# Kernel tuning notes

Measured on AMD Instinct MI355X. Metric: run time of the kernel, lower is better.

The kernel has to match this reference:

```python
import jax, jax.numpy as jnp
import numpy as np

COLLAPSE_FRAC = 4  # collapse F // 4 lowest-weight faces (target_size = 3/4 * F)


def setup_inputs() -> dict:
    key = jax.random.key(0)
    k1, k2, k3 = jax.random.split(key, 3)
    B, F, C, K = 8, 8192, 256, 4
    features = jax.random.normal(k1, (B, F, C), dtype=jnp.float32)
    adjacency = jax.random.randint(k2, (B, F, 3), 0, F).astype(jnp.int32)
    ring_k = jax.random.randint(k3, (B, F, K), 0, F).astype(jnp.int32)
    return {"features": features, "adjacency": adjacency, "ring_k": ring_k}


def _pool(features, adjacency, ring_k):
    # features:  [B, F, C] float   per-face features
    # adjacency: [B, F, 3] int     3 neighboring faces of each triangle
    # ring_k:    [B, F, K] int     k-ring neighborhood used for collapse weights
    B, F, C = features.shape
    K = ring_k.shape[-1]
    # ring-aggregated saliency weight per face (compute_weights analogue)
    rf = jnp.take_along_axis(
        features, ring_k.reshape(B, F * K)[:, :, None], axis=1
    ).reshape(B, F, K, C)                      # [B, F, K, C]
    w = jnp.linalg.norm(rf.mean(axis=2), axis=-1)  # [B, F]

    # select lowest-weight faces to collapse (idx/sorted analogue)
    P = F // COLLAPSE_FRAC
    _, collapse_idx = jax.lax.top_k(-w, P)      # [B, P]

    # gather the 3 region neighbors and the collapsed face features
    neighbors = jnp.take_along_axis(adjacency, collapse_idx[:, :, None], axis=1)  # [B, P, 3]
    cf = jnp.take_along_axis(features, collapse_idx[:, :, None], axis=1)          # [B, P, C]

    # scatter collapsed-face features into their 3 adjacent faces (update_features analogue)
    offs = (jnp.arange(B, dtype=jnp.int32) * F)[:, None, None]   # [B, 1, 1]
    seg = (neighbors + offs).reshape(-1)                          # [B*P*3]
    vals = jnp.broadcast_to(cf[:, :, None, :] / 3.0, (B, P, 3, C)).reshape(-1, C)
    scat = jax.ops.segment_sum(vals, seg, num_segments=B * F).reshape(B, F, C)
    cnt = jax.ops.segment_sum(
        jnp.ones(seg.shape, jnp.float32), seg, num_segments=B * F
    ).reshape(B, F, 1)
    merged = (features + scat) / (1.0 + cnt)

    # erase collapsed faces (erased / update_faces analogue; static shape, mask instead of compaction)
    erase_flat = (collapse_idx + offs[:, :, 0]).reshape(-1)
    keep = (
        jnp.ones((B * F,), jnp.float32).at[erase_flat].set(0.0).reshape(B, F, 1)
    )
    return merged * keep


def reference(features, adjacency, ring_k):
    return _pool(features, adjacency, ring_k)
```

## Files before the change

kernel.cpp:

```cpp
#include <hip/hip_runtime.h>
#include <stdint.h>

#define B 8
#define F 8192
#define C 256
#define K 4
#define P (F / 4)
#define CAP 16
#define NB 4096
#define BF (B * F)
#define CCAP 1024

typedef float f32x4 __attribute__((ext_vector_type(4)));

__device__ __forceinline__ int binOf(float v, float lo, float scale) {
    int bin = (int)((v - lo) * scale);
    return bin < 0 ? 0 : (bin > NB - 1 ? NB - 1 : bin);
}

__global__ __launch_bounds__(256) void kW(const float* __restrict__ feat,
                                          const int* __restrict__ ring,
                                          float* __restrict__ w,
                                          int* __restrict__ cnt,
                                          int* __restrict__ flag) {
    const int b     = blockIdx.x & 7;
    const int inner = blockIdx.x >> 3;
    const int wid   = b * F + inner * 4 + (threadIdx.x >> 6);
    const int lane  = threadIdx.x & 63;

    const int rbase = wid * K;
    const int r0 = ring[rbase + 0], r1 = ring[rbase + 1];
    const int r2 = ring[rbase + 2], r3 = ring[rbase + 3];
    const float4* f4 = (const float4*)feat;
    const size_t base = (size_t)b * F;
    const int    CW   = C / 4;
    const float4 v0 = f4[(base + r0) * CW + lane];
    const float4 v1 = f4[(base + r1) * CW + lane];
    const float4 v2 = f4[(base + r2) * CW + lane];
    const float4 v3 = f4[(base + r3) * CW + lane];

    float4 a;
    a.x = (v0.x + v1.x) + (v2.x + v3.x);
    a.y = (v0.y + v1.y) + (v2.y + v3.y);
    a.z = (v0.z + v1.z) + (v2.z + v3.z);
    a.w = (v0.w + v1.w) + (v2.w + v3.w);
    float s = (a.x * a.x + a.y * a.y + a.z * a.z + a.w * a.w) * 0.0625f;
#pragma unroll
    for (int off = 32; off > 0; off >>= 1) s += __shfl_down(s, off, 64);
    if (lane == 0) {
        w[wid]    = s;
        cnt[wid]  = 0;
        flag[wid] = 0;
    }
}

__global__ __launch_bounds__(256) void kFS(const float* __restrict__ w,
                                           const int* __restrict__ adj,
                                           int* __restrict__ flag,
                                           int* __restrict__ cnt,
                                           int* __restrict__ srcs) {
    __shared__ int h[NB];
    __shared__ unsigned long long carr[CCAP];
    __shared__ unsigned int redmn[4], redmx[4];
    __shared__ int wsum[4];
    __shared__ unsigned int slo, shi;
    __shared__ int sT, sR, scnt;
    const int g    = blockIdx.x;
    const int b    = g >> 5;
    const int gg   = g & 31;
    const int t    = threadIdx.x;
    const int lane = t & 63, wv = t >> 6;

    if (t == 0) scnt = 0;
    for (int i = t; i < NB; i += 256) h[i] = 0;

    float val[32];
    unsigned int mn = 0xFFFFFFFFu, mx = 0u;
#pragma unroll
    for (int k = 0; k < 32; ++k) {
        val[k] = w[b * F + k * 256 + t];
        const unsigned int u = __float_as_uint(val[k]);
        mn = mn < u ? mn : u;
        mx = mx > u ? mx : u;
    }
#pragma unroll
    for (int off = 32; off > 0; off >>= 1) {
        const unsigned int o1 = __shfl_xor(mn, off, 64); mn = mn < o1 ? mn : o1;
        const unsigned int o2 = __shfl_xor(mx, off, 64); mx = mx > o2 ? mx : o2;
    }
    if (lane == 0) { redmn[wv] = mn; redmx[wv] = mx; }
    __syncthreads();
    if (t == 0) {
        unsigned int a = redmn[0], c = redmx[0];
        for (int i = 1; i < 4; ++i) {
            a = a < redmn[i] ? a : redmn[i];
            c = c > redmx[i] ? c : redmx[i];
        }
        slo = a; shi = c;
    }
    __syncthreads();
    const float lo    = __uint_as_float(slo);
    const float hi    = __uint_as_float(shi);
    const float scale = (float)(NB - 2) / fmaxf(hi - lo, 1e-30f);

#pragma unroll
    for (int k = 0; k < 32; ++k) atomicAdd(&h[binOf(val[k], lo, scale)], 1);
    __syncthreads();

    int s = 0;
#pragma unroll
    for (int i = 0; i < 16; ++i) s += h[t * 16 + i];
    int incl = s;
#pragma unroll
    for (int off = 1; off < 64; off <<= 1) {
        const int u = __shfl_up(incl, off, 64);
        if (lane >= off) incl += u;
    }
    if (lane == 63) wsum[wv] = incl;
    __syncthreads();
    int add = 0;
    for (int i = 0; i < wv; ++i) add += wsum[i];
    const int inclT = incl + add;
    const int exclT = inclT - s;
    if (P - 1 >= exclT && P - 1 < inclT) {
        int c = exclT;
#pragma unroll
        for (int i = 0; i < 16; ++i) {
            const int bin = t * 16 + i;
            const int hv  = h[bin];
            if (P - 1 < c + hv) { sT = bin; sR = P - c; break; }
            c += hv;
        }
    }
    __syncthreads();
    const int T = sT, R = sR;

    const float myv = val[gg];
    const int face  = b * F + gg * 256 + t;
    if (binOf(myv, lo, scale) < T) {
        flag[face] = 1;
#pragma unroll
        for (int j = 0; j < 3; ++j) {
            const int n    = adj[(size_t)face * 3 + j];
            const int tgt  = b * F + n;
            const int slot = atomicAdd(&cnt[tgt], 1);
            if (slot < CAP) srcs[(size_t)tgt * CAP + slot] = face;
        }
    }

    if (gg == 0) {
#pragma unroll
        for (int k = 0; k < 32; ++k) {
            if (binOf(val[k], lo, scale) == T) {
                const int pos = atomicAdd(&scnt, 1);
                if (pos < CCAP)
                    carr[pos] = ((unsigned long long)__float_as_uint(val[k]) << 32) |
                                (uint32_t)(k * 256 + t);
            }
        }
        __syncthreads();
        const int n = scnt < CCAP ? scnt : CCAP;
        for (int i = t; i < n; i += 256) {
            const unsigned long long my = carr[i];
            int rank = 0;
            for (int j = 0; j < n; ++j) rank += (carr[j] < my) ? 1 : 0;
            if (rank < R) {
                const int tt = b * F + (int)(uint32_t)my;
                flag[tt] = 1;
#pragma unroll
                for (int j = 0; j < 3; ++j) {
                    const int nb   = adj[(size_t)tt * 3 + j];
                    const int tgt  = b * F + nb;
                    const int slot = atomicAdd(&cnt[tgt], 1);
                    if (slot < CAP) srcs[(size_t)tgt * CAP + slot] = tt;
                }
            }
        }
    }
}

__global__ __launch_bounds__(256) void kG(const float* __restrict__ feat,
                                          const int* __restrict__ cnt,
                                          const int* __restrict__ flag,
                                          const int* __restrict__ srcs,
                                          float* __restrict__ out) {
    const int b     = blockIdx.x & 7;
    const int inner = blockIdx.x >> 3;
    const int wid   = b * F + inner * 4 + (threadIdx.x >> 6);
    const int lane  = threadIdx.x & 63;
    f32x4* drow = (f32x4*)(out + (size_t)wid * C);

    if (flag[wid]) {
        f32x4 z = {0.f, 0.f, 0.f, 0.f};
        __builtin_nontemporal_store(z, &drow[lane]);
        return;
    }
    const int m  = cnt[wid];
    const int mm = m < CAP ? m : CAP;

    float4 acc = ((const float4*)(feat + (size_t)wid * C))[lane];
    if (mm > 0) {
        const int sidx = (lane < CAP) ? srcs[(size_t)wid * CAP + lane] : 0;
        const float inv3 = 1.0f / 3.0f;
        for (int i = 0; i < mm; ++i) {
            const int s = __shfl(sidx, i, 64);
            const float4 v = ((const float4*)(feat + (size_t)s * C))[lane];
            acc.x += v.x * inv3; acc.y += v.y * inv3;
            acc.z += v.z * inv3; acc.w += v.w * inv3;
        }
    }
    const float inv = 1.0f / (1.0f + (float)m);
    f32x4 r;
    r.x = acc.x * inv; r.y = acc.y * inv;
    r.z = acc.z * inv; r.w = acc.w * inv;
    __builtin_nontemporal_store(r, &drow[lane]);
}

extern "C" void kernel_launch(void* const* d_in, const int* in_sizes, int n_in,
                              void* d_out, int out_size, void* d_ws, size_t ws_size,
                              hipStream_t stream) {
    const float* feat = (const float*)d_in[0];
    const int*   adj  = (const int*)d_in[1];
    const int*   ring = (const int*)d_in[2];
    float* out = (float*)d_out;

    float* w    = (float*)d_ws;
    int*   cnt  = (int*)(w + BF);
    int*   flag = cnt + BF;
    int*   srcs = flag + BF;

    kW  <<<BF / 4, 256, 0, stream>>>(feat, ring, w, cnt, flag);
    kFS <<<BF / 256, 256, 0, stream>>>(w, adj, flag, cnt, srcs);
    kG  <<<BF / 4, 256, 0, stream>>>(feat, cnt, flag, srcs, out);
}
```

Measured before the change: 156.6 us.

## Fuse selection and gather into one kernel with block-local shared-memory scatter lists

Merges the threshold-selection kernel and the gather kernel into one kernel. Each of 256 blocks recomputes the batch histogram and threshold, collects the full list of collapsed faces in shared memory, and builds per-face source lists only for its own 256-face slice. This removes the global cnt/flag/srcs arrays, their global atomics, and one launch. In exchange every block redundantly scans the whole batch and walks all collapsed faces' adjacency. The gather now runs on only 256 blocks, with each wave looping over 64 faces, which lowers parallelism for the memory-bound phase. The histogram bin count is also halved so the histogram buffer can be reused for the collapse list.

```diff
diff --git a/kernel.cpp b/kernel.cpp
--- a/kernel.cpp
+++ b/kernel.cpp
@@ -7,7 +7,7 @@
 #define K 4
 #define P (F / 4)
 #define CAP 16
-#define NB 4096
+#define NB 2048
 #define BF (B * F)
 #define CCAP 1024
 
@@ -20,9 +20,7 @@
 
 __global__ __launch_bounds__(256) void kW(const float* __restrict__ feat,
                                           const int* __restrict__ ring,
-                                          float* __restrict__ w,
-                                          int* __restrict__ cnt,
-                                          int* __restrict__ flag) {
+                                          float* __restrict__ w) {
     const int b     = blockIdx.x & 7;
     const int inner = blockIdx.x >> 3;
     const int wid   = b * F + inner * 4 + (threadIdx.x >> 6);
@@ -47,32 +45,32 @@
     float s = (a.x * a.x + a.y * a.y + a.z * a.z + a.w * a.w) * 0.0625f;
 #pragma unroll
     for (int off = 32; off > 0; off >>= 1) s += __shfl_down(s, off, 64);
-    if (lane == 0) {
-        w[wid]    = s;
-        cnt[wid]  = 0;
-        flag[wid] = 0;
-    }
-}
-
-__global__ __launch_bounds__(256) void kFS(const float* __restrict__ w,
-                                           const int* __restrict__ adj,
-                                           int* __restrict__ flag,
-                                           int* __restrict__ cnt,
-                                           int* __restrict__ srcs) {
+    if (lane == 0) w[wid] = s;
+}
+
+__global__ __launch_bounds__(256) void kM(const float* __restrict__ feat,
+                                          const float* __restrict__ w,
+                                          const int* __restrict__ adj,
+                                          float* __restrict__ out) {
     __shared__ int h[NB];
     __shared__ unsigned long long carr[CCAP];
+    __shared__ int lists[256 * CAP];
+    __shared__ int lcnt[256];
+    __shared__ int sflag[256];
     __shared__ unsigned int redmn[4], redmx[4];
     __shared__ int wsum[4];
     __shared__ unsigned int slo, shi;
-    __shared__ int sT, sR, scnt;
+    __shared__ int sT, sR, sncol, sncar;
+
     const int g    = blockIdx.x;
-    const int b    = g >> 5;
-    const int gg   = g & 31;
+    const int b    = g & 7;
+    const int gg   = g >> 3;
     const int t    = threadIdx.x;
     const int lane = t & 63, wv = t >> 6;
 
-    if (t == 0) scnt = 0;
-    for (int i = t; i < NB; i += 256) h[i] = 0;
+    if (t == 0) { sncol = 0; sncar = 0; }
+    lcnt[t]  = 0;
+    sflag[t] = 0;
 
     float val[32];
     unsigned int mn = 0xFFFFFFFFu, mx = 0u;
@@ -89,6 +87,7 @@
         const unsigned int o2 = __shfl_xor(mx, off, 64); mx = mx > o2 ? mx : o2;
     }
     if (lane == 0) { redmn[wv] = mn; redmx[wv] = mx; }
+    for (int i = t; i < NB; i += 256) h[i] = 0;
     __syncthreads();
     if (t == 0) {
         unsigned int a = redmn[0], c = redmx[0];
@@ -106,10 +105,9 @@
 #pragma unroll
     for (int k = 0; k < 32; ++k) atomicAdd(&h[binOf(val[k], lo, scale)], 1);
     __syncthreads();
-
     int s = 0;
 #pragma unroll
-    for (int i = 0; i < 16; ++i) s += h[t * 16 + i];
+    for (int i = 0; i < 8; ++i) s += h[t * 8 + i];
     int incl = s;
 #pragma unroll
     for (int off = 1; off < 64; off <<= 1) {
@@ -125,8 +123,8 @@
     if (P - 1 >= exclT && P - 1 < inclT) {
         int c = exclT;
 #pragma unroll
-        for (int i = 0; i < 16; ++i) {
-            const int bin = t * 16 + i;
+        for (int i = 0; i < 8; ++i) {
+            const int bin = t * 8 + i;
             const int hv  = h[bin];
             if (P - 1 < c + hv) { sT = bin; sR = P - c; break; }
             c += hv;
@@ -134,86 +132,79 @@
     }
     __syncthreads();
     const int T = sT, R = sR;
-
-    const float myv = val[gg];
-    const int face  = b * F + gg * 256 + t;
-    if (binOf(myv, lo, scale) < T) {
-        flag[face] = 1;
+    int* col = h;
+
+#pragma unroll
+    for (int k = 0; k < 32; ++k) {
+        const int bin = binOf(val[k], lo, scale);
+        if (bin < T) {
+            const int pos = atomicAdd(&sncol, 1);
+            col[pos] = k * 256 + t;
+            if (k == gg) sflag[t] = 1;
+        } else if (bin == T) {
+            const int pos = atomicAdd(&sncar, 1);
+            if (pos < CCAP)
+                carr[pos] = ((unsigned long long)__float_as_uint(val[k]) << 32) |
+                            (uint32_t)(k * 256 + t);
+        }
+    }
+    __syncthreads();
+    const int n = sncar < CCAP ? sncar : CCAP;
+    for (int i = t; i < n; i += 256) {
+        const unsigned long long my = carr[i];
+        int rank = 0;
+        for (int j = 0; j < n; ++j) rank += (carr[j] < my) ? 1 : 0;
+        if (rank < R) {
+            const int f   = (int)(uint32_t)my;
+            const int pos = atomicAdd(&sncol, 1);
+            col[pos] = f;
+            if ((f >> 8) == gg) sflag[f & 255] = 1;
+        }
+    }
+    __syncthreads();
+
+    const int ncol = sncol < 2048 ? sncol : 2048;
+    for (int i = t; i < ncol; i += 256) {
+        const int c    = col[i];
+        const size_t a = (size_t)(b * F + c) * 3;
 #pragma unroll
         for (int j = 0; j < 3; ++j) {
-            const int n    = adj[(size_t)face * 3 + j];
-            const int tgt  = b * F + n;
-            const int slot = atomicAdd(&cnt[tgt], 1);
-            if (slot < CAP) srcs[(size_t)tgt * CAP + slot] = face;
-        }
-    }
-
-    if (gg == 0) {
-#pragma unroll
-        for (int k = 0; k < 32; ++k) {
-            if (binOf(val[k], lo, scale) == T) {
-                const int pos = atomicAdd(&scnt, 1);
-                if (pos < CCAP)
-                    carr[pos] = ((unsigned long long)__float_as_uint(val[k]) << 32) |
-                                (uint32_t)(k * 256 + t);
+            const int tgt = adj[a + j];
+            if ((tgt >> 8) == gg) {
+                const int fl  = tgt & 255;
+                const int pos = atomicAdd(&lcnt[fl], 1);
+                if (pos < CAP) lists[fl * CAP + pos] = c;
             }
         }
-        __syncthreads();
-        const int n = scnt < CCAP ? scnt : CCAP;
-        for (int i = t; i < n; i += 256) {
-            const unsigned long long my = carr[i];
-            int rank = 0;
-            for (int j = 0; j < n; ++j) rank += (carr[j] < my) ? 1 : 0;
-            if (rank < R) {
-                const int tt = b * F + (int)(uint32_t)my;
-                flag[tt] = 1;
-#pragma unroll
-                for (int j = 0; j < 3; ++j) {
-                    const int nb   = adj[(size_t)tt * 3 + j];
-                    const int tgt  = b * F + nb;
-                    const int slot = atomicAdd(&cnt[tgt], 1);
-                    if (slot < CAP) srcs[(size_t)tgt * CAP + slot] = tt;
-                }
-            }
-        }
-    }
-}
-
-__global__ __launch_bounds__(256) void kG(const float* __restrict__ feat,
-                                          const int* __restrict__ cnt,
-                                          const int* __restrict__ flag,
-                                          const int* __restrict__ srcs,
-                                          float* __restrict__ out) {
-    const int b     = blockIdx.x & 7;
-    const int inner = blockIdx.x >> 3;
-    const int wid   = b * F + inner * 4 + (threadIdx.x >> 6);
-    const int lane  = threadIdx.x & 63;
-    f32x4* drow = (f32x4*)(out + (size_t)wid * C);
-
-    if (flag[wid]) {
-        f32x4 z = {0.f, 0.f, 0.f, 0.f};
-        __builtin_nontemporal_store(z, &drow[lane]);
-        return;
-    }
-    const int m  = cnt[wid];
-    const int mm = m < CAP ? m : CAP;
-
-    float4 acc = ((const float4*)(feat + (size_t)wid * C))[lane];
-    if (mm > 0) {
-        const int sidx = (lane < CAP) ? srcs[(size_t)wid * CAP + lane] : 0;
-        const float inv3 = 1.0f / 3.0f;
+    }
+    __syncthreads();
+
+    const int CW = C / 4;
+    const float inv3 = 1.0f / 3.0f;
+    for (int j = 0; j < 64; ++j) {
+        const int fl = wv * 64 + j;
+        const int fg = b * F + gg * 256 + fl;
+        f32x4* drow = (f32x4*)(out + (size_t)fg * C);
+        if (sflag[fl]) {
+            f32x4 z = {0.f, 0.f, 0.f, 0.f};
+            __builtin_nontemporal_store(z, &drow[lane]);
+            continue;
+        }
+        const int m  = lcnt[fl];
+        const int mm = m < CAP ? m : CAP;
+        float4 acc = ((const float4*)(feat + (size_t)fg * C))[lane];
         for (int i = 0; i < mm; ++i) {
-            const int s = __shfl(sidx, i, 64);
-            const float4 v = ((const float4*)(feat + (size_t)s * C))[lane];
+            const int c = lists[fl * CAP + i];
+            const float4 v = ((const float4*)(feat + (size_t)(b * F + c) * C))[lane];
             acc.x += v.x * inv3; acc.y += v.y * inv3;
             acc.z += v.z * inv3; acc.w += v.w * inv3;
         }
-    }
-    const float inv = 1.0f / (1.0f + (float)m);
-    f32x4 r;
-    r.x = acc.x * inv; r.y = acc.y * inv;
-    r.z = acc.z * inv; r.w = acc.w * inv;
-    __builtin_nontemporal_store(r, &drow[lane]);
+        const float inv = 1.0f / (1.0f + (float)m);
+        f32x4 r;
+        r.x = acc.x * inv; r.y = acc.y * inv;
+        r.z = acc.z * inv; r.w = acc.w * inv;
+        __builtin_nontemporal_store(r, &drow[lane]);
+    }
 }
 
 extern "C" void kernel_launch(void* const* d_in, const int* in_sizes, int n_in,
@@ -224,12 +215,8 @@
     const int*   ring = (const int*)d_in[2];
     float* out = (float*)d_out;
 
-    float* w    = (float*)d_ws;
-    int*   cnt  = (int*)(w + BF);
-    int*   flag = cnt + BF;
-    int*   srcs = flag + BF;
-
-    kW  <<<BF / 4, 256, 0, stream>>>(feat, ring, w, cnt, flag);
-    kFS <<<BF / 256, 256, 0, stream>>>(w, adj, flag, cnt, srcs);
-    kG  <<<BF / 4, 256, 0, stream>>>(feat, cnt, flag, srcs, out);
-}
+    float* w = (float*)d_ws;
+
+    kW<<<BF / 4, 256, 0, stream>>>(feat, ring, w);
+    kM<<<256, 256, 0, stream>>>(feat, w, adj, out);
+}
```

Result: slower. 165.3 us (+5.5%).
